# Kernel tuning notes

Hardware: AMD Instinct MI355X
Metric: run time of the kernel (lower is better)

Reference implementation:

```python
import jax, jax.numpy as jnp
import numpy as np
from jax import lax

N = 4096      # network_size
B = 1024      # batch
AVG_DEG = 6.0 # scale-free preferential attachment adds ~3 edges/node (undirected)
N_STEPS = 10


def setup_inputs() -> dict:
    key = jax.random.key(0)
    k_in, k_adj = jax.random.split(key)
    external_input = jax.random.normal(k_in, (B, N), dtype=jnp.float32)
    # symmetric binary adjacency with average degree ~6 (stand-in for scale-free topology)
    a = jax.random.bernoulli(k_adj, AVG_DEG / N, (N, N))
    connectivity = jnp.maximum(a, a.T).astype(jnp.float32)
    connectivity = connectivity * (1.0 - jnp.eye(N, dtype=jnp.float32))  # no self-loops
    membrane_potentials = jnp.zeros((N,), dtype=jnp.float32)  # nn.Parameter init zeros
    thresholds = jnp.ones((N,), dtype=jnp.float32)            # nn.Parameter init ones
    refractory_periods = jnp.zeros((N,), dtype=jnp.float32)   # nn.Parameter init zeros
    return {
        "external_input": external_input,
        "connectivity": connectivity,
        "membrane_potentials": membrane_potentials,
        "thresholds": thresholds,
        "refractory_periods": refractory_periods,
    }


def reference(external_input, connectivity, membrane_potentials, thresholds, refractory_periods):
    b, n = external_input.shape
    v0 = membrane_potentials[None, :] + external_input          # [B, N]
    s0 = jnp.zeros((b, n), dtype=external_input.dtype)          # spikes

    def step(carry, _):
        v, s, refr = carry
        v = v + 0.1 * (s @ connectivity)                         # network input
        mask = (v > thresholds[None, :]) & (refr == 0.0)[None, :]
        new_s = mask.astype(v.dtype)
        v = jnp.where(mask, 0.0, v)                              # reset on spike
        refr = jnp.where(jnp.any(mask, axis=0), 3.0, refr)       # set refractory
        refr = jnp.clip(refr - 1.0, 0.0, 10.0)                   # decay
        v = v * 0.95                                             # leak
        return (v, new_s, refr), None

    (_, spikes, _), _ = lax.scan(step, (v0, s0, refractory_periods), None, length=N_STEPS)
    return spikes
```

## Files before the change

kernel.cpp:

```cpp
#include <hip/hip_runtime.h>
#include <stdint.h>

#define N_ 4096
#define B_ 1024
#define ROWB 512
#define NSTEPS_ 10
#define DEG_SLOTS 40
#define UNR 16
#define PAD_E ((uint32_t)(N_ * ROWB))
#define NBLK 256
#define NCTR 16
#define FLAGI 512

#define OFF_BAR  0
#define OFF_DEG  8192
#define OFF_NBR  24576
#define OFF_SEXP 679936
#define SEXP_BUF ((N_ + 1) * ROWB)

__global__ __launch_bounds__(256) void build_k(const float* __restrict__ C,
                                               uint32_t* __restrict__ deg,
                                               uint32_t* __restrict__ nbr,
                                               uint32_t* __restrict__ bar,
                                               uint32_t* __restrict__ pad0,
                                               uint32_t* __restrict__ pad1) {
    __shared__ uint32_t cnt;
    int tid = threadIdx.x;
    int n = blockIdx.x;
    if (n == 0) { for (int i = tid; i < 1056; i += 256) bar[i] = 0u; }
    else if (n == 1) { if (tid < 128) pad0[tid] = 0u; }
    else if (n == 2) { if (tid < 128) pad1[tid] = 0u; }
    if (tid == 0) cnt = 0;
    __syncthreads();
    const float4* row = (const float4*)(C + (size_t)n * N_);
    for (int j4 = tid; j4 < N_ / 4; j4 += 256) {
        float4 v = row[j4];
        int base = j4 * 4;
        #pragma unroll
        for (int q = 0; q < 4; ++q) {
            float f = (q == 0) ? v.x : (q == 1) ? v.y : (q == 2) ? v.z : v.w;
            if (f != 0.0f) {
                uint32_t p = atomicAdd(&cnt, 1u);
                uint32_t m = (uint32_t)(base + q);
                if (p < DEG_SLOTS) nbr[n * DEG_SLOTS + p] = m * (uint32_t)ROWB;
            }
        }
    }
    __syncthreads();
    uint32_t c = min(cnt, (uint32_t)DEG_SLOTS);
    if (tid == 0) deg[n] = c;
    if (tid < DEG_SLOTS && (uint32_t)tid >= c)
        nbr[n * DEG_SLOTS + tid] = PAD_E;
}

__device__ __forceinline__ void gbar(uint32_t* bar, uint32_t phase) {
    __syncthreads();
    int tid = threadIdx.x, bid = blockIdx.x;
    if (tid == 0)
        __hip_atomic_fetch_add(&bar[(bid & (NCTR - 1)) * 32], 1u,
                               __ATOMIC_RELAXED, __HIP_MEMORY_SCOPE_AGENT);
    if (bid == 0) {
        if (tid < NCTR) {
            uint32_t tgt = (NBLK / NCTR) * phase;
            while (__hip_atomic_load(&bar[tid * 32], __ATOMIC_RELAXED,
                                     __HIP_MEMORY_SCOPE_AGENT) < tgt)
                __builtin_amdgcn_s_sleep(2);
        }
        __syncthreads();
        if (tid == 0)
            __hip_atomic_store(&bar[FLAGI], phase,
                               __ATOMIC_RELAXED, __HIP_MEMORY_SCOPE_AGENT);
    }
    if (tid == 0) {
        while (__hip_atomic_load(&bar[FLAGI], __ATOMIC_RELAXED,
                                 __HIP_MEMORY_SCOPE_AGENT) < phase)
            __builtin_amdgcn_s_sleep(2);
        (void)__hip_atomic_load(&bar[FLAGI], __ATOMIC_ACQUIRE,
                                __HIP_MEMORY_SCOPE_AGENT);
    }
    __syncthreads();
}

__global__ __launch_bounds__(1024, 4) void persist_k(const float* __restrict__ ext,
                                                     const float* __restrict__ memb,
                                                     const float* __restrict__ thr,
                                                     const float* __restrict__ refr_in,
                                                     const uint32_t* __restrict__ deg,
                                                     const uint32_t* __restrict__ nbr,
                                                     unsigned char* __restrict__ sExp,
                                                     float* __restrict__ out,
                                                     uint32_t* bar) {
    __shared__ uint32_t s_nbr[16 * DEG_SLOTS];
    __shared__ unsigned char bt[16][528];

    int bid = blockIdx.x;
    int n0 = bid * 16;
    int tid = threadIdx.x;
    int wv = tid >> 6, lane = tid & 63;
    int n = n0 + wv;
    int bbatch = lane * 16;
    int bbn = lane * 8;

    if (tid < 16 * DEG_SLOTS) s_nbr[tid] = nbr[(size_t)n0 * DEG_SLOTS + tid];
    __syncthreads();

    float tn = thr[n];
    float r  = refr_in[n];
    uint32_t dg = __builtin_amdgcn_readfirstlane(deg[n]);
    const uint32_t* lst = &s_nbr[wv * DEG_SLOTS];

    float v[16];
    {
        float mb = memb[n];
        #pragma unroll
        for (int i = 0; i < 16; ++i)
            v[i] = __fadd_rn(mb, ext[(size_t)(bbatch + i) * N_ + n]);
    }

    uint32_t nib0 = 0, nib1 = 0;

    {
        uint32_t nb = (r != 0.0f) ? 0u : 1u;
        nib0 = 0; nib1 = 0;
        #pragma unroll
        for (int i = 0; i < 16; ++i) {
            int sp = (v[i] > tn) && nb;
            if (i < 8) nib0 |= (uint32_t)sp << (4 * i);
            else       nib1 |= (uint32_t)sp << (4 * (i - 8));
            v[i] = __fmul_rn(sp ? 0.0f : v[i], 0.95f);
        }
        unsigned long long p0 = (unsigned long long)nib0 | ((unsigned long long)nib1 << 32);
        __hip_atomic_store((unsigned long long*)(sExp + (size_t)n * ROWB + bbn), p0,
                           __ATOMIC_RELAXED, __HIP_MEMORY_SCOPE_AGENT);
        int any = (__ballot((nib0 | nib1) != 0) != 0ull);
        r = any ? 3.0f : r;
        r = fminf(fmaxf(__fadd_rn(r, -1.0f), 0.0f), 10.0f);
    }
    gbar(bar, 1);

    unsigned char* sprev = sExp;
    unsigned char* snext = sExp + (size_t)SEXP_BUF;
    for (int s = 1; s < NSTEPS_; ++s) {
        uint32_t nb = (r != 0.0f) ? 0u : 1u;
        uint2 accA = make_uint2(0u, 0u), accB = make_uint2(0u, 0u);
        uint2 accC = make_uint2(0u, 0u), accD = make_uint2(0u, 0u);
        #pragma unroll
        for (int j = 0; j < 8; ++j) {
            uint32_t e = lst[j];
            uint2 d2 = *(const uint2*)(sprev + e + bbn);
            accA.x += d2.x; accA.y += d2.y;
        }
        #pragma unroll
        for (int j = 8; j < 16; ++j) {
            uint32_t e = lst[j];
            uint2 d2 = *(const uint2*)(sprev + e + bbn);
            accB.x += d2.x; accB.y += d2.y;
        }
        if (dg > 16) {
            #pragma unroll
            for (int j = 16; j < 31; ++j) {
                uint32_t e = lst[j];
                uint2 d2 = *(const uint2*)(sprev + e + bbn);
                accC.x += d2.x; accC.y += d2.y;
            }
        }
        if (dg > 31) {
            #pragma unroll
            for (int j = 31; j < 40; ++j) {
                uint32_t e = lst[j];
                uint2 d2 = *(const uint2*)(sprev + e + bbn);
                accD.x += d2.x; accD.y += d2.y;
            }
        }
        uint32_t newn0 = 0, newn1 = 0;
        #pragma unroll
        for (int h = 0; h < 2; ++h) {
            uint32_t a = h ? accA.y : accA.x;
            uint32_t b = h ? accB.y : accB.x;
            uint32_t c = h ? accC.y : accC.x;
            uint32_t d = h ? accD.y : accD.x;
            #pragma unroll
            for (int i = 0; i < 8; ++i) {
                uint32_t sh = 4u * i;
                uint32_t cc = ((a >> sh) & 15u) + ((b >> sh) & 15u) +
                              ((c >> sh) & 15u) + ((d >> sh) & 15u);
                int bi = h * 8 + i;
                float vv = __fadd_rn(v[bi], __fmul_rn(0.1f, (float)cc));
                int sp = (vv > tn) && nb;
                if (h == 0) newn0 |= (uint32_t)sp << sh;
                else        newn1 |= (uint32_t)sp << sh;
                if (s < NSTEPS_ - 1)
                    v[bi] = __fmul_rn(sp ? 0.0f : vv, 0.95f);
            }
        }
        nib0 = newn0; nib1 = newn1;
        if (s < NSTEPS_ - 1) {
            unsigned long long p0 = (unsigned long long)nib0 | ((unsigned long long)nib1 << 32);
            __hip_atomic_store((unsigned long long*)(snext + (size_t)n * ROWB + bbn), p0,
                               __ATOMIC_RELAXED, __HIP_MEMORY_SCOPE_AGENT);
            int any = (__ballot((nib0 | nib1) != 0) != 0ull);
            r = any ? 3.0f : r;
            r = fminf(fmaxf(__fadd_rn(r, -1.0f), 0.0f), 10.0f);
            gbar(bar, (uint32_t)s + 1);
        }
        unsigned char* t = sprev; sprev = snext; snext = t;
    }

    *(uint2*)&bt[wv][bbn] = make_uint2(nib0, nib1);
    __syncthreads();
    #pragma unroll
    for (int p = 0; p < 4; ++p) {
        int i = tid + p * 1024;
        int rrow = i >> 2, c4 = (i & 3) * 4;
        uint32_t shl = (uint32_t)(rrow & 1) * 4u;
        int col = rrow >> 1;
        float4 o;
        o.x = (float)((bt[c4 + 0][col] >> shl) & 1u);
        o.y = (float)((bt[c4 + 1][col] >> shl) & 1u);
        o.z = (float)((bt[c4 + 2][col] >> shl) & 1u);
        o.w = (float)((bt[c4 + 3][col] >> shl) & 1u);
        *(float4*)&out[(size_t)rrow * N_ + n0 + c4] = o;
    }
}

extern "C" void kernel_launch(void* const* d_in, const int* in_sizes, int n_in,
                              void* d_out, int out_size, void* d_ws, size_t ws_size,
                              hipStream_t stream) {
    const float* ext     = (const float*)d_in[0];
    const float* C       = (const float*)d_in[1];
    const float* memb    = (const float*)d_in[2];
    const float* thr     = (const float*)d_in[3];
    const float* refr_in = (const float*)d_in[4];

    char* ws = (char*)d_ws;
    uint32_t* bar    = (uint32_t*)(ws + OFF_BAR);
    uint32_t* deg    = (uint32_t*)(ws + OFF_DEG);
    uint32_t* nbr    = (uint32_t*)(ws + OFF_NBR);
    unsigned char* sExp = (unsigned char*)(ws + OFF_SEXP);
    float*    out    = (float*)d_out;

    build_k<<<dim3(N_), dim3(256), 0, stream>>>(
        C, deg, nbr, bar,
        (uint32_t*)(sExp + (size_t)N_ * ROWB),
        (uint32_t*)(sExp + (size_t)SEXP_BUF + (size_t)N_ * ROWB));

    void* args[] = {(void*)&ext, (void*)&memb, (void*)&thr, (void*)&refr_in,
                    (void*)&deg, (void*)&nbr, (void*)&sExp, (void*)&out,
                    (void*)&bar};
    hipLaunchCooperativeKernel((const void*)persist_k, dim3(NBLK), dim3(1024),
                               args, 0, stream);
}
```

Measured before the change: 128.9 us.

## Fuse adjacency list construction into persistent kernel and use SWAR nibble summation

Removes the separate 4096-block build kernel and instead has each wave of the persistent kernel scan its own connectivity row into shared-memory neighbor lists, leaving only a tiny barrier-reset kernel before launch. This cuts a launch and the global write and read of deg/nbr arrays. Pad-row zeroing also moves into the persistent kernel. The per-step count extraction now sums even and odd nibbles of all four accumulators in packed byte lanes instead of extracting each nibble separately. The connectivity scan is now serial within only 256 blocks, and shared-memory atomic contention per wave may add latency.

```diff
diff --git a/kernel.cpp b/kernel.cpp
--- a/kernel.cpp
+++ b/kernel.cpp
@@ -6,51 +6,17 @@
 #define ROWB 512
 #define NSTEPS_ 10
 #define DEG_SLOTS 40
-#define UNR 16
 #define PAD_E ((uint32_t)(N_ * ROWB))
 #define NBLK 256
 #define NCTR 16
 #define FLAGI 512
 
 #define OFF_BAR  0
-#define OFF_DEG  8192
-#define OFF_NBR  24576
-#define OFF_SEXP 679936
+#define OFF_SEXP 8192
 #define SEXP_BUF ((N_ + 1) * ROWB)
 
-__global__ __launch_bounds__(256) void build_k(const float* __restrict__ C,
-                                               uint32_t* __restrict__ deg,
-                                               uint32_t* __restrict__ nbr,
-                                               uint32_t* __restrict__ bar,
-                                               uint32_t* __restrict__ pad0,
-                                               uint32_t* __restrict__ pad1) {
-    __shared__ uint32_t cnt;
-    int tid = threadIdx.x;
-    int n = blockIdx.x;
-    if (n == 0) { for (int i = tid; i < 1056; i += 256) bar[i] = 0u; }
-    else if (n == 1) { if (tid < 128) pad0[tid] = 0u; }
-    else if (n == 2) { if (tid < 128) pad1[tid] = 0u; }
-    if (tid == 0) cnt = 0;
-    __syncthreads();
-    const float4* row = (const float4*)(C + (size_t)n * N_);
-    for (int j4 = tid; j4 < N_ / 4; j4 += 256) {
-        float4 v = row[j4];
-        int base = j4 * 4;
-        #pragma unroll
-        for (int q = 0; q < 4; ++q) {
-            float f = (q == 0) ? v.x : (q == 1) ? v.y : (q == 2) ? v.z : v.w;
-            if (f != 0.0f) {
-                uint32_t p = atomicAdd(&cnt, 1u);
-                uint32_t m = (uint32_t)(base + q);
-                if (p < DEG_SLOTS) nbr[n * DEG_SLOTS + p] = m * (uint32_t)ROWB;
-            }
-        }
-    }
-    __syncthreads();
-    uint32_t c = min(cnt, (uint32_t)DEG_SLOTS);
-    if (tid == 0) deg[n] = c;
-    if (tid < DEG_SLOTS && (uint32_t)tid >= c)
-        nbr[n * DEG_SLOTS + tid] = PAD_E;
+__global__ void initbar_k(uint32_t* __restrict__ bar) {
+    for (int i = threadIdx.x; i < 1056; i += 256) bar[i] = 0u;
 }
 
 __device__ __forceinline__ void gbar(uint32_t* bar, uint32_t phase) {
@@ -82,15 +48,15 @@
 }
 
 __global__ __launch_bounds__(1024, 4) void persist_k(const float* __restrict__ ext,
+                                                     const float* __restrict__ C,
                                                      const float* __restrict__ memb,
                                                      const float* __restrict__ thr,
                                                      const float* __restrict__ refr_in,
-                                                     const uint32_t* __restrict__ deg,
-                                                     const uint32_t* __restrict__ nbr,
                                                      unsigned char* __restrict__ sExp,
                                                      float* __restrict__ out,
                                                      uint32_t* bar) {
     __shared__ uint32_t s_nbr[16 * DEG_SLOTS];
+    __shared__ uint32_t s_cnt[16];
     __shared__ unsigned char bt[16][528];
 
     int bid = blockIdx.x;
@@ -101,12 +67,49 @@
     int bbatch = lane * 16;
     int bbn = lane * 8;
 
-    if (tid < 16 * DEG_SLOTS) s_nbr[tid] = nbr[(size_t)n0 * DEG_SLOTS + tid];
+    if (tid < 16) s_cnt[tid] = 0u;
+    __syncthreads();
+    {
+        const float4* row = (const float4*)(C + (size_t)n * N_);
+        #pragma unroll
+        for (int c = 0; c < 4; ++c) {
+            float4 d[4];
+            #pragma unroll
+            for (int u = 0; u < 4; ++u)
+                d[u] = row[lane + (c * 4 + u) * 64];
+            #pragma unroll
+            for (int u = 0; u < 4; ++u) {
+                int base = (lane + (c * 4 + u) * 64) * 4;
+                #pragma unroll
+                for (int q = 0; q < 4; ++q) {
+                    float f = (q == 0) ? d[u].x : (q == 1) ? d[u].y
+                            : (q == 2) ? d[u].z : d[u].w;
+                    if (f != 0.0f) {
+                        uint32_t p = atomicAdd(&s_cnt[wv], 1u);
+                        if (p < DEG_SLOTS)
+                            s_nbr[wv * DEG_SLOTS + p] = (uint32_t)(base + q) * ROWB;
+                    }
+                }
+            }
+        }
+    }
+    if (bid == 1 && tid < 64) {
+        __hip_atomic_store((unsigned long long*)(sExp + (size_t)N_ * ROWB) + tid, 0ull,
+                           __ATOMIC_RELAXED, __HIP_MEMORY_SCOPE_AGENT);
+    } else if (bid == 2 && tid < 64) {
+        __hip_atomic_store((unsigned long long*)(sExp + (size_t)SEXP_BUF + (size_t)N_ * ROWB) + tid,
+                           0ull, __ATOMIC_RELAXED, __HIP_MEMORY_SCOPE_AGENT);
+    }
+    __syncthreads();
+    for (int i = tid; i < 16 * DEG_SLOTS; i += 1024) {
+        int rw = i / DEG_SLOTS, sl = i - rw * DEG_SLOTS;
+        if ((uint32_t)sl >= min(s_cnt[rw], (uint32_t)DEG_SLOTS)) s_nbr[i] = PAD_E;
+    }
     __syncthreads();
 
     float tn = thr[n];
     float r  = refr_in[n];
-    uint32_t dg = __builtin_amdgcn_readfirstlane(deg[n]);
+    uint32_t dg = __builtin_amdgcn_readfirstlane(min(s_cnt[wv], (uint32_t)DEG_SLOTS));
     const uint32_t* lst = &s_nbr[wv * DEG_SLOTS];
 
     float v[16];
@@ -121,7 +124,6 @@
 
     {
         uint32_t nb = (r != 0.0f) ? 0u : 1u;
-        nib0 = 0; nib1 = 0;
         #pragma unroll
         for (int i = 0; i < 16; ++i) {
             int sp = (v[i] > tn) && nb;
@@ -179,19 +181,28 @@
             uint32_t b = h ? accB.y : accB.x;
             uint32_t c = h ? accC.y : accC.x;
             uint32_t d = h ? accD.y : accD.x;
-            #pragma unroll
-            for (int i = 0; i < 8; ++i) {
-                uint32_t sh = 4u * i;
-                uint32_t cc = ((a >> sh) & 15u) + ((b >> sh) & 15u) +
-                              ((c >> sh) & 15u) + ((d >> sh) & 15u);
-                int bi = h * 8 + i;
-                float vv = __fadd_rn(v[bi], __fmul_rn(0.1f, (float)cc));
-                int sp = (vv > tn) && nb;
-                if (h == 0) newn0 |= (uint32_t)sp << sh;
-                else        newn1 |= (uint32_t)sp << sh;
-                if (s < NSTEPS_ - 1)
-                    v[bi] = __fmul_rn(sp ? 0.0f : vv, 0.95f);
-            }
+            uint32_t sumE = (a & 0x0F0F0F0Fu) + (b & 0x0F0F0F0Fu) +
+                            (c & 0x0F0F0F0Fu) + (d & 0x0F0F0F0Fu);
+            uint32_t sumO = ((a >> 4) & 0x0F0F0F0Fu) + ((b >> 4) & 0x0F0F0F0Fu) +
+                            ((c >> 4) & 0x0F0F0F0Fu) + ((d >> 4) & 0x0F0F0F0Fu);
+            uint32_t nh = 0;
+            #pragma unroll
+            for (int k = 0; k < 4; ++k) {
+                float ce = (float)((sumE >> (8 * k)) & 255u);
+                float co = (float)((sumO >> (8 * k)) & 255u);
+                int be = h * 8 + 2 * k, bo = be + 1;
+                float ve = __fadd_rn(v[be], __fmul_rn(0.1f, ce));
+                float vo = __fadd_rn(v[bo], __fmul_rn(0.1f, co));
+                int se = (ve > tn) && nb;
+                int so = (vo > tn) && nb;
+                nh |= (uint32_t)se << (4 * (2 * k));
+                nh |= (uint32_t)so << (4 * (2 * k + 1));
+                if (s < NSTEPS_ - 1) {
+                    v[be] = __fmul_rn(se ? 0.0f : ve, 0.95f);
+                    v[bo] = __fmul_rn(so ? 0.0f : vo, 0.95f);
+                }
+            }
+            if (h == 0) newn0 = nh; else newn1 = nh;
         }
         nib0 = newn0; nib1 = newn1;
         if (s < NSTEPS_ - 1) {
@@ -234,19 +245,13 @@
 
     char* ws = (char*)d_ws;
     uint32_t* bar    = (uint32_t*)(ws + OFF_BAR);
-    uint32_t* deg    = (uint32_t*)(ws + OFF_DEG);
-    uint32_t* nbr    = (uint32_t*)(ws + OFF_NBR);
     unsigned char* sExp = (unsigned char*)(ws + OFF_SEXP);
     float*    out    = (float*)d_out;
 
-    build_k<<<dim3(N_), dim3(256), 0, stream>>>(
-        C, deg, nbr, bar,
-        (uint32_t*)(sExp + (size_t)N_ * ROWB),
-        (uint32_t*)(sExp + (size_t)SEXP_BUF + (size_t)N_ * ROWB));
-
-    void* args[] = {(void*)&ext, (void*)&memb, (void*)&thr, (void*)&refr_in,
-                    (void*)&deg, (void*)&nbr, (void*)&sExp, (void*)&out,
-                    (void*)&bar};
+    initbar_k<<<dim3(1), dim3(256), 0, stream>>>(bar);
+
+    void* args[] = {(void*)&ext, (void*)&C, (void*)&memb, (void*)&thr,
+                    (void*)&refr_in, (void*)&sExp, (void*)&out, (void*)&bar};
     hipLaunchCooperativeKernel((const void*)persist_k, dim3(NBLK), dim3(1024),
                                args, 0, stream);
 }
```

After: 131.4 us. No clear change (+2.0%).
